# Kernel tuning notes

Hardware: AMD Instinct MI355X
Metric: run time of the kernel (lower is better)

## Reference

```python
import jax, jax.numpy as jnp
import numpy as np

N = 100000      # nodes
E = 3200000     # edges (avg degree 32)
NFEAT = 512
NHID = 256
NCLASS = 40
NLAYERS = 8
T1 = 5
T2 = 5
G1 = 1
G2 = 1
BETA = 0.5      # weight_beta
LAMDA = 0.5
ALPHA = 0.1
EPS = 1e-5


def ortho_trans(weight, T, groups):
    """Newton-Schulz orthogonalization (Ortho_Trans.forward)."""
    g = groups
    Z = weight.reshape(g, weight.shape[0] // g, -1)          # [g, d, k]
    Zc = Z - Z.mean(axis=-1, keepdims=True)
    S = jnp.einsum('gik,gjk->gij', Zc, Zc)                   # covariance [g, d, d]
    eye = jnp.eye(S.shape[-1], dtype=S.dtype)
    S = S + EPS * eye
    norm_S = jnp.sqrt(jnp.sum(S * S, axis=(1, 2), keepdims=True))  # fro norm
    S = S / norm_S
    B0 = jnp.broadcast_to(eye, S.shape)

    def body(B, _):
        B3 = B @ B @ B                                       # matrix_power3
        return 1.5 * B - 0.5 * (B3 @ S), None                # baddbmm(1.5,B,-0.5,B3,S)

    Bt, _ = jax.lax.scan(body, B0, None, length=T)
    W = (Bt @ Zc) / jnp.sqrt(norm_S)
    return W.reshape(weight.shape)


def setup_inputs() -> dict:
    key = jax.random.key(0)
    ks = jax.random.split(key, 8)
    stdv = 1.0 / np.sqrt(NHID)
    return {
        'x': jax.random.normal(ks[0], (N, NFEAT), dtype=jnp.float32),
        'edge_src': jax.random.randint(ks[1], (E,), 0, N, dtype=jnp.int32),
        'edge_dst': jax.random.randint(ks[2], (E,), 0, N, dtype=jnp.int32),
        'edge_weight': jax.random.uniform(ks[3], (E,), dtype=jnp.float32),
        'W0': jax.random.normal(ks[4], (NHID, NFEAT), dtype=jnp.float32) * 0.05,
        'b0': jnp.zeros((NHID,), dtype=jnp.float32),
        'convW': jax.random.uniform(ks[5], (NLAYERS, NHID, NHID), dtype=jnp.float32,
                                    minval=-stdv, maxval=stdv),
        'W1': jax.random.normal(ks[6], (NCLASS, NHID), dtype=jnp.float32) * 0.05,
        'b1': jnp.zeros((NCLASS,), dtype=jnp.float32),
    }


def reference(x, edge_src, edge_dst, edge_weight, W0, b0, convW, W1, b1):
    # fcs[0].weight is orthogonalized at init (Ortho=True)
    W0o = ortho_trans(W0, T1, G1)
    h = jax.nn.relu(x @ W0o.T + b0)                          # [N, NHID]
    h0 = h
    I = jnp.eye(NHID, dtype=h.dtype)
    ls = jnp.arange(1, NLAYERS + 1, dtype=h.dtype)

    def layer(h, inp):
        W, l = inp
        theta = jnp.log(LAMDA / l + 1.0)
        # sparse spmm: hi = adj @ h
        msgs = edge_weight[:, None] * h[edge_src]            # [E, NHID]
        hi = jax.ops.segment_sum(msgs, edge_dst, num_segments=N)
        support = (1.0 - ALPHA) * hi + ALPHA * h0            # variant=False -> r == support
        we = BETA * W + (1.0 - BETA) * I
        t = ortho_trans(we, T2, G2)
        out = jax.nn.relu(theta * (support @ t) + (1.0 - theta) * support)
        return out, None

    h, _ = jax.lax.scan(layer, h, (convW, ls))
    logits = h @ W1.T + b1
    return jax.nn.log_softmax(logits, axis=1)
```

## Files before the change

### kernel.cpp

```cpp
#include <hip/hip_runtime.h>
#include <math.h>

#define NNODES 100000
#define NEDGE  3200000
#define NF     512
#define NH     256
#define NC     40
#define NLAY   8
#define EPSV   1e-5f

typedef __attribute__((ext_vector_type(8))) short short8;
typedef __attribute__((ext_vector_type(4))) float floatx4;



__device__ __forceinline__ float block_sum_256(float v) {
    __shared__ float sb[8];
    #pragma unroll
    for (int off = 32; off; off >>= 1) v += __shfl_down(v, off, 64);
    if ((threadIdx.x & 63) == 0) sb[threadIdx.x >> 6] = v;
    __syncthreads();
    return sb[0] + sb[1] + sb[2] + sb[3];
}

__device__ __forceinline__ unsigned short bf16_rte(float a) {
    unsigned int u = __float_as_uint(a);
    return (unsigned short)((u + 0x7fffu + ((u >> 16) & 1u)) >> 16);
}
__device__ __forceinline__ unsigned int pack_bf2(float a, float b) {
    unsigned int ua = __float_as_uint(a), ub = __float_as_uint(b);
    ua = (ua + 0x7fffu + ((ua >> 16) & 1u)) >> 16;
    ub = (ub + 0x7fffu + ((ub >> 16) & 1u)) & 0xffff0000u;
    return ua | ub;
}


__global__ void k_hist(const int* __restrict__ dst, int* __restrict__ counts, int n) {
    int i = blockIdx.x * 256 + threadIdx.x;
    if (i < n) atomicAdd(&counts[dst[i]], 1);
}

__global__ void k_scan1(const int* __restrict__ in, int* __restrict__ out,
                        int* __restrict__ bsum, int n) {
    __shared__ int s[1024];
    int t = threadIdx.x, g = blockIdx.x * 1024 + t;
    int v = (g < n) ? in[g] : 0;
    s[t] = v; __syncthreads();
    for (int off = 1; off < 1024; off <<= 1) {
        int u = (t >= off) ? s[t - off] : 0;
        __syncthreads();
        s[t] += u;
        __syncthreads();
    }
    if (g < n) out[g] = s[t] - v;
    if (t == 1023) bsum[blockIdx.x] = s[1023];
}

__global__ void k_scan2(int* __restrict__ bsum, int nb) {
    __shared__ int s[128];
    int t = threadIdx.x;
    int v = (t < nb) ? bsum[t] : 0;
    s[t] = v; __syncthreads();
    for (int off = 1; off < 128; off <<= 1) {
        int u = (t >= off) ? s[t - off] : 0;
        __syncthreads();
        s[t] += u;
        __syncthreads();
    }
    if (t < nb) bsum[t] = s[t] - v;
}

__global__ void k_scan3(int* __restrict__ out, const int* __restrict__ bsum, int n) {
    int g = blockIdx.x * 1024 + threadIdx.x;
    if (g < n) out[g] += bsum[blockIdx.x];
}

__global__ void k_scatter(const int* __restrict__ src, const int* __restrict__ dst,
                          const float* __restrict__ w, const int* __restrict__ rstart,
                          int* __restrict__ cursor, unsigned int* __restrict__ epack, int n) {
    int i = blockIdx.x * 256 + threadIdx.x;
    if (i < n) {
        int d = dst[i];
        int pos = rstart[d] + atomicAdd(&cursor[d], 1);
        unsigned int wb = bf16_rte(w[i]) & 0x7FFFu;
        epack[pos] = ((unsigned int)src[i] << 15) | wb;
    }
}


__global__ void k_zc0(const float* __restrict__ W0, float* __restrict__ Zc0) {
    int r = blockIdx.x, t = threadIdx.x;
    float a = W0[r * NF + t];
    float b = W0[r * NF + 256 + t];
    float mean = block_sum_256(a + b) * (1.0f / 512.0f);
    Zc0[r * NF + t]       = a - mean;
    Zc0[r * NF + 256 + t] = b - mean;
}

__global__ void k_zcC(const float* __restrict__ convW, float* __restrict__ ZcC) {
    int g = blockIdx.x >> 8, r = blockIdx.x & 255, t = threadIdx.x;
    float v = 0.5f * convW[((size_t)g * NH + r) * NH + t] + ((r == t) ? 0.5f : 0.0f);
    float mean = block_sum_256(v) * (1.0f / 256.0f);
    ZcC[((size_t)g * NH + r) * NH + t] = v - mean;
}

__global__ __launch_bounds__(256) void k_gram(const float* __restrict__ Zc0,
                                              const float* __restrict__ ZcC,
                                              float* __restrict__ S) {
    const int b = blockIdx.z;
    const float* A = (b == 0) ? Zc0 : (ZcC + (size_t)(b - 1) * 65536);
    const int K = (b == 0) ? 512 : 256;
    const int r0 = blockIdx.y * 64, c0 = blockIdx.x * 64;
    __shared__ float As[32][76], Bs[32][76];
    const int t = threadIdx.x, tx = t & 15, ty = t >> 4;
    const int lr = t >> 2, lk = (t & 3) * 4;
    float acc[4][4] = {};
    for (int k0 = 0; k0 < K; k0 += 32) {
        float4 a0 = *(const float4*)(A + (size_t)(r0 + lr) * K + k0 + lk);
        float4 a1 = *(const float4*)(A + (size_t)(r0 + lr) * K + k0 + lk + 16);
        As[lk + 0][lr] = a0.x; As[lk + 1][lr] = a0.y; As[lk + 2][lr] = a0.z; As[lk + 3][lr] = a0.w;
        As[lk + 16][lr] = a1.x; As[lk + 17][lr] = a1.y; As[lk + 18][lr] = a1.z; As[lk + 19][lr] = a1.w;
        float4 b0 = *(const float4*)(A + (size_t)(c0 + lr) * K + k0 + lk);
        float4 b1 = *(const float4*)(A + (size_t)(c0 + lr) * K + k0 + lk + 16);
        Bs[lk + 0][lr] = b0.x; Bs[lk + 1][lr] = b0.y; Bs[lk + 2][lr] = b0.z; Bs[lk + 3][lr] = b0.w;
        Bs[lk + 16][lr] = b1.x; Bs[lk + 17][lr] = b1.y; Bs[lk + 18][lr] = b1.z; Bs[lk + 19][lr] = b1.w;
        __syncthreads();
        #pragma unroll
        for (int kk = 0; kk < 32; kk++) {
            float a[4], bb[4];
            *(float4*)&a[0]  = *(const float4*)&As[kk][ty * 4];
            *(float4*)&bb[0] = *(const float4*)&Bs[kk][tx * 4];
            #pragma unroll
            for (int i = 0; i < 4; i++)
                #pragma unroll
                for (int j = 0; j < 4; j++) acc[i][j] = fmaf(a[i], bb[j], acc[i][j]);
        }
        __syncthreads();
    }
    #pragma unroll
    for (int i = 0; i < 4; i++)
        #pragma unroll
        for (int j = 0; j < 4; j++) {
            int r = r0 + ty * 4 + i, c = c0 + tx * 4 + j;
            float v = acc[i][j];
            if (r == c) v += EPSV;
            S[(size_t)b * 65536 + r * NH + c] = v;
        }
}

__global__ void k_fro(const float* __restrict__ S, float* __restrict__ scales) {
    __shared__ float sb[8];
    const int b = blockIdx.x, t = threadIdx.x;
    const float* p = S + (size_t)b * 65536;
    float s = 0.f;
    for (int i = t; i < 65536; i += 256) { float v = p[i]; s = fmaf(v, v, s); }
    #pragma unroll
    for (int off = 32; off; off >>= 1) s += __shfl_down(s, off, 64);
    if ((t & 63) == 0) sb[t >> 6] = s;
    __syncthreads();
    if (t == 0) {
        float nrm = sqrtf(sb[0] + sb[1] + sb[2] + sb[3]);
        scales[b]      = 1.0f / nrm;
        scales[16 + b] = rsqrtf(nrm);
    }
}

__global__ void k_initB1(const float* __restrict__ S, const float* __restrict__ scales,
                         float* __restrict__ B) {
    int i = blockIdx.x * 256 + threadIdx.x;
    int b = i >> 16, m = i & 65535;
    float v = -0.5f * scales[b] * S[i];
    if ((m >> 8) == (m & 255)) v += 1.5f;
    B[i] = v;
}

__global__ __launch_bounds__(256) void k_ns_pair(const float* __restrict__ Bb,
                                                 const float* __restrict__ Smat,
                                                 float* __restrict__ T1b,
                                                 float* __restrict__ T2b) {
    const int b = blockIdx.z;
    const int bb = (b < 9) ? b : b - 9;
    const float* A  = Bb + (size_t)bb * 65536;
    const float* Bm = (b < 9) ? A : (Smat + (size_t)bb * 65536);
    float* C = (b < 9) ? (T1b + (size_t)bb * 65536) : (T2b + (size_t)bb * 65536);
    const int r0 = blockIdx.y * 64, c0 = blockIdx.x * 64;
    __shared__ float As[32][76], Bs[32][76];
    const int t = threadIdx.x, tx = t & 15, ty = t >> 4;
    const int lr = t >> 2, lk = (t & 3) * 4;
    const int bk = t >> 3, bc = (t & 7) * 8;
    float acc[4][4] = {};
    for (int k0 = 0; k0 < 256; k0 += 32) {
        float4 a0 = *(const float4*)(A + (size_t)(r0 + lr) * 256 + k0 + lk);
        float4 a1 = *(const float4*)(A + (size_t)(r0 + lr) * 256 + k0 + lk + 16);
        As[lk + 0][lr] = a0.x; As[lk + 1][lr] = a0.y; As[lk + 2][lr] = a0.z; As[lk + 3][lr] = a0.w;
        As[lk + 16][lr] = a1.x; As[lk + 17][lr] = a1.y; As[lk + 18][lr] = a1.z; As[lk + 19][lr] = a1.w;
        float4 b0 = *(const float4*)(Bm + (size_t)(k0 + bk) * 256 + c0 + bc);
        float4 b1 = *(const float4*)(Bm + (size_t)(k0 + bk) * 256 + c0 + bc + 4);
        *(float4*)&Bs[bk][bc]     = b0;
        *(float4*)&Bs[bk][bc + 4] = b1;
        __syncthreads();
        #pragma unroll
        for (int kk = 0; kk < 32; kk++) {
            float a[4], bb2[4];
            *(float4*)&a[0]   = *(const float4*)&As[kk][ty * 4];
            *(float4*)&bb2[0] = *(const float4*)&Bs[kk][tx * 4];
            #pragma unroll
            for (int i = 0; i < 4; i++)
                #pragma unroll
                for (int j = 0; j < 4; j++) acc[i][j] = fmaf(a[i], bb2[j], acc[i][j]);
        }
        __syncthreads();
    }
    #pragma unroll
    for (int i = 0; i < 4; i++)
        #pragma unroll
        for (int j = 0; j < 4; j++)
            C[(size_t)(r0 + ty * 4 + i) * 256 + c0 + tx * 4 + j] = acc[i][j];
}

__global__ __launch_bounds__(256) void k_small_nn(const float* __restrict__ A0,
                                                  const float* __restrict__ B0,
                                                  float* __restrict__ C0,
                                                  int sA, int sB, int sC,
                                                  int K, int Ncols, int mode,
                                                  const float* __restrict__ scale) {
    const int b = blockIdx.z;
    const float* A = A0 + (size_t)b * sA;
    const float* Bm = B0 + (size_t)b * sB;
    float* C = C0 + (size_t)b * sC;
    const int r0 = blockIdx.y * 64, c0 = blockIdx.x * 64;
    __shared__ float As[32][76], Bs[32][76];
    const int t = threadIdx.x, tx = t & 15, ty = t >> 4;
    const int lr = t >> 2, lk = (t & 3) * 4;
    const int bk = t >> 3, bc = (t & 7) * 8;
    float acc[4][4] = {};
    for (int k0 = 0; k0 < K; k0 += 32) {
        float4 a0 = *(const float4*)(A + (size_t)(r0 + lr) * K + k0 + lk);
        float4 a1 = *(const float4*)(A + (size_t)(r0 + lr) * K + k0 + lk + 16);
        As[lk + 0][lr] = a0.x; As[lk + 1][lr] = a0.y; As[lk + 2][lr] = a0.z; As[lk + 3][lr] = a0.w;
        As[lk + 16][lr] = a1.x; As[lk + 17][lr] = a1.y; As[lk + 18][lr] = a1.z; As[lk + 19][lr] = a1.w;
        float4 b0 = *(const float4*)(Bm + (size_t)(k0 + bk) * Ncols + c0 + bc);
        float4 b1 = *(const float4*)(Bm + (size_t)(k0 + bk) * Ncols + c0 + bc + 4);
        *(float4*)&Bs[bk][bc]     = b0;
        *(float4*)&Bs[bk][bc + 4] = b1;
        __syncthreads();
        #pragma unroll
        for (int kk = 0; kk < 32; kk++) {
            float a[4], bb[4];
            *(float4*)&a[0]  = *(const float4*)&As[kk][ty * 4];
            *(float4*)&bb[0] = *(const float4*)&Bs[kk][tx * 4];
            #pragma unroll
            for (int i = 0; i < 4; i++)
                #pragma unroll
                for (int j = 0; j < 4; j++) acc[i][j] = fmaf(a[i], bb[j], acc[i][j]);
        }
        __syncthreads();
    }
    #pragma unroll
    for (int i = 0; i < 4; i++)
        #pragma unroll
        for (int j = 0; j < 4; j++) {
            size_t idx = (size_t)(r0 + ty * 4 + i) * Ncols + c0 + tx * 4 + j;
            if (mode == 1) C[idx] = 1.5f * C[idx] - 0.5f * scale[b] * acc[i][j];
            else C[idx] = scale[b] * acc[i][j];
        }
}


__global__ void k_prepM(const float* __restrict__ tbuf, unsigned short* __restrict__ Mpack) {
    int idx = blockIdx.x * 256 + threadIdx.x;
    int lane = idx & 63;
    int tg   = (idx >> 6) & 15;
    int s    = (idx >> 10) & 1;
    int c    = (idx >> 11) & 3;
    int l    = idx >> 13;
    float theta = logf(0.5f / (float)(l + 1) + 1.0f);
    float mtheta = 1.0f - theta;
    int n  = tg * 16 + (lane & 15);
    int k0 = c * 64 + s * 32 + (lane >> 4) * 8;
    const float* T = tbuf + (size_t)l * 65536;
    unsigned short o[8];
    #pragma unroll
    for (int j = 0; j < 8; j++) {
        int kp = k0 + j;
        int kn = (kp & 0xC0) | ((kp & 3) << 4) | ((kp >> 2) & 15);
        float v = theta * T[(size_t)kn * 256 + n] + ((kn == n) ? mtheta : 0.0f);
        o[j] = bf16_rte(v);
    }
    *(uint4*)(Mpack + (size_t)idx * 8) = *(uint4*)o;
}

__global__ void k_prepW0(const float* __restrict__ W0o, unsigned short* __restrict__ Wpack) {
    int idx = blockIdx.x * 256 + threadIdx.x;
    int lane = idx & 63;
    int tg   = (idx >> 6) & 15;
    int s    = (idx >> 10) & 1;
    int c    = idx >> 11;
    int n  = tg * 16 + (lane & 15);
    int k0 = c * 64 + s * 32 + (lane >> 4) * 8;
    const float* p = W0o + (size_t)n * NF + k0;
    unsigned short o[8];
    #pragma unroll
    for (int j = 0; j < 8; j++) o[j] = bf16_rte(p[j]);
    *(uint4*)(Wpack + (size_t)idx * 8) = *(uint4*)o;
}



__global__ __launch_bounds__(256) void k_fc0_mfma(const float* __restrict__ X,
                                                  const unsigned short* __restrict__ Wp,
                                                  const float* __restrict__ bias,
                                                  unsigned char* __restrict__ h0u8,
                                                  float* __restrict__ h0scale) {
    __shared__ unsigned short Bs[2][16][64][8];
    __shared__ int rmax[64];
    const int t = threadIdx.x, lane = t & 63, w = t >> 6;
    const int q = lane >> 4, m = lane & 15;
    const int r0 = blockIdx.x * 64;
    if (t < 64) rmax[t] = 0;
    floatx4 acc[4][4] = {};
    for (int c = 0; c < 8; c++) {
        const uint4* src = (const uint4*)(Wp + (size_t)c * 16384);
        uint4* dst = (uint4*)&Bs[0][0][0][0];
        #pragma unroll
        for (int i = 0; i < 8; i++) dst[t + 256 * i] = src[t + 256 * i];
        __syncthreads();
        #pragma unroll
        for (int s = 0; s < 2; s++) {
            short8 afr[4];
            #pragma unroll
            for (int i = 0; i < 4; i++) {
                int row = r0 + i * 16 + m; if (row > NNODES - 1) row = NNODES - 1;
                const float* p = X + (size_t)row * NF + c * 64 + s * 32 + q * 8;
                float4 xa = *(const float4*)p;
                float4 xb = *(const float4*)(p + 4);
                uint4 af;
                af.x = pack_bf2(xa.x, xa.y); af.y = pack_bf2(xa.z, xa.w);
                af.z = pack_bf2(xb.x, xb.y); af.w = pack_bf2(xb.z, xb.w);
                afr[i] = *(short8*)&af;
            }
            #pragma unroll
            for (int tg = 0; tg < 4; tg++) {
                short8 bfr = *(const short8*)&Bs[s][w * 4 + tg][lane][0];
                #pragma unroll
                for (int i = 0; i < 4; i++)
                    acc[i][tg] = __builtin_amdgcn_mfma_f32_16x16x32_bf16(afr[i], bfr, acc[i][tg], 0, 0, 0);
            }
        }
        __syncthreads();
    }
    #pragma unroll
    for (int tg = 0; tg < 4; tg++) {
        float bv = bias[w * 64 + tg * 16 + m];
        #pragma unroll
        for (int i = 0; i < 4; i++)
            #pragma unroll
            for (int r = 0; r < 4; r++)
                acc[i][tg][r] = fmaxf(acc[i][tg][r] + bv, 0.f);
    }
    #pragma unroll
    for (int i = 0; i < 4; i++)
        #pragma unroll
        for (int r = 0; r < 4; r++) {
            float mx = fmaxf(fmaxf(acc[i][0][r], acc[i][1][r]),
                             fmaxf(acc[i][2][r], acc[i][3][r]));
            mx = fmaxf(mx, __shfl_xor(mx, 1));
            mx = fmaxf(mx, __shfl_xor(mx, 2));
            mx = fmaxf(mx, __shfl_xor(mx, 4));
            mx = fmaxf(mx, __shfl_xor(mx, 8));
            if (m == 0) atomicMax(&rmax[i * 16 + q * 4 + r], __float_as_int(mx));
        }
    __syncthreads();
    #pragma unroll
    for (int i = 0; i < 4; i++)
        #pragma unroll
        for (int r = 0; r < 4; r++) {
            int row = r0 + i * 16 + q * 4 + r;
            if (row >= NNODES) continue;
            float rm = __int_as_float(rmax[i * 16 + q * 4 + r]);
            float qs = rm > 0.f ? 255.0f / rm : 0.f;
            unsigned int b0 = (unsigned int)fmaf(acc[i][0][r], qs, 0.5f);
            unsigned int b1 = (unsigned int)fmaf(acc[i][1][r], qs, 0.5f);
            unsigned int b2 = (unsigned int)fmaf(acc[i][2][r], qs, 0.5f);
            unsigned int b3 = (unsigned int)fmaf(acc[i][3][r], qs, 0.5f);
            *(unsigned int*)(h0u8 + (size_t)row * NH + w * 64 + m * 4) =
                b0 | (b1 << 8) | (b2 << 16) | (b3 << 24);
        }
    if (t < 64 && r0 + t < NNODES)
        h0scale[r0 + t] = __int_as_float(rmax[t]) * (1.0f / 255.0f);
}


__global__ __launch_bounds__(256) void k_spmm(const int* __restrict__ rstart,
                                              const int* __restrict__ counts,
                                              const unsigned int* __restrict__ epack,
                                              const unsigned char* __restrict__ hu8,
                                              const float* __restrict__ hscale,
                                              const unsigned char* __restrict__ h0u8,
                                              const float* __restrict__ h0scale,
                                              unsigned short* __restrict__ supbf) {
    __shared__ int2 se[4][64];
    const int wv = threadIdx.x >> 6, lane = threadIdx.x & 63;
    const int node = blockIdx.x * 4 + wv;
    const int start = rstart[node], deg = counts[node];
    float a0 = 0.f, a1 = 0.f, a2 = 0.f, a3 = 0.f;
    for (int base = 0; base < deg; base += 64) {
        int j = base + lane;
        if (j < deg) {
            unsigned int u = epack[start + j];
            int s = (int)(u >> 15);
            float wt = __uint_as_float((u & 0x7FFFu) << 16);
            se[wv][lane] = make_int2(s, __float_as_int(wt * hscale[s] * 0.9f));
        }
        int mm = deg - base; if (mm > 64) mm = 64;
        int e = 0;
        for (; e + 8 <= mm; e += 8) {
            float ww[8]; unsigned int g[8];
            #pragma unroll
            for (int u = 0; u < 8; u++) {
                int2 ed = se[wv][e + u];
                ww[u] = __int_as_float(ed.y);
                g[u] = *(const unsigned int*)(hu8 + ((size_t)ed.x << 8) + (lane << 2));
            }
            #pragma unroll
            for (int u = 0; u < 8; u++) {
                a0 = fmaf(ww[u], (float)(g[u] & 0xFFu), a0);
                a1 = fmaf(ww[u], (float)((g[u] >> 8) & 0xFFu), a1);
                a2 = fmaf(ww[u], (float)((g[u] >> 16) & 0xFFu), a2);
                a3 = fmaf(ww[u], (float)(g[u] >> 24), a3);
            }
        }
        for (; e < mm; e++) {
            int2 ed = se[wv][e];
            float ww = __int_as_float(ed.y);
            unsigned int g = *(const unsigned int*)(hu8 + ((size_t)ed.x << 8) + (lane << 2));
            a0 = fmaf(ww, (float)(g & 0xFFu), a0);
            a1 = fmaf(ww, (float)((g >> 8) & 0xFFu), a1);
            a2 = fmaf(ww, (float)((g >> 16) & 0xFFu), a2);
            a3 = fmaf(ww, (float)(g >> 24), a3);
        }
    }
    unsigned int rg = *(const unsigned int*)(h0u8 + ((size_t)node << 8) + (lane << 2));
    float rs = h0scale[node] * 0.1f;
    float o0 = fmaf(rs, (float)(rg & 0xFFu), a0);
    float o1 = fmaf(rs, (float)((rg >> 8) & 0xFFu), a1);
    float o2 = fmaf(rs, (float)((rg >> 16) & 0xFFu), a2);
    float o3 = fmaf(rs, (float)(rg >> 24), a3);
    uint2 ov;
    ov.x = pack_bf2(o0, o1);
    ov.y = pack_bf2(o2, o3);
    *(uint2*)(supbf + ((size_t)node << 8) + (lane << 2)) = ov;
}


__global__ __launch_bounds__(256) void k_gemm_layer(const unsigned short* __restrict__ Sbf,
                                                    const unsigned short* __restrict__ Mp,
                                                    unsigned char* __restrict__ out_u8,
                                                    float* __restrict__ out_scale,
                                                    unsigned short* __restrict__ out_bf) {
    __shared__ int rmax[64];
    const int t = threadIdx.x, lane = t & 63, w = t >> 6;
    const int q = lane >> 4, m = lane & 15;
    const int r0 = blockIdx.x * 64;
    if (t < 64) rmax[t] = 0;
    floatx4 acc[4][4] = {};
    #pragma unroll
    for (int c = 0; c < 4; c++) {
        #pragma unroll
        for (int s = 0; s < 2; s++) {
            short8 afr[4];
            #pragma unroll
            for (int i = 0; i < 4; i++) {
                int row = r0 + i * 16 + m; if (row > NNODES - 1) row = NNODES - 1;
                afr[i] = *(const short8*)(Sbf + (size_t)row * NH + c * 64 + s * 32 + q * 8);
            }
            #pragma unroll
            for (int tg = 0; tg < 4; tg++) {
                short8 bfr = *(const short8*)(Mp + (size_t)c * 16384 + s * 8192
                                              + (w * 4 + tg) * 512 + lane * 8);
                #pragma unroll
                for (int i = 0; i < 4; i++)
                    acc[i][tg] = __builtin_amdgcn_mfma_f32_16x16x32_bf16(afr[i], bfr, acc[i][tg], 0, 0, 0);
            }
        }
    }
    #pragma unroll
    for (int i = 0; i < 4; i++)
        #pragma unroll
        for (int tg = 0; tg < 4; tg++)
            #pragma unroll
            for (int r = 0; r < 4; r++)
                acc[i][tg][r] = fmaxf(acc[i][tg][r], 0.f);

    if (out_bf) {
        #pragma unroll
        for (int i = 0; i < 4; i++)
            #pragma unroll
            for (int tg = 0; tg < 4; tg++) {
                int col = w * 64 + tg * 16 + m;
                #pragma unroll
                for (int r = 0; r < 4; r++) {
                    int row = r0 + i * 16 + q * 4 + r;
                    if (row >= NNODES) continue;
                    out_bf[(size_t)row * NH + col] = bf16_rte(acc[i][tg][r]);
                }
            }
        return;
    }
    __syncthreads();
    #pragma unroll
    for (int i = 0; i < 4; i++)
        #pragma unroll
        for (int r = 0; r < 4; r++) {
            float mx = fmaxf(fmaxf(acc[i][0][r], acc[i][1][r]),
                             fmaxf(acc[i][2][r], acc[i][3][r]));
            mx = fmaxf(mx, __shfl_xor(mx, 1));
            mx = fmaxf(mx, __shfl_xor(mx, 2));
            mx = fmaxf(mx, __shfl_xor(mx, 4));
            mx = fmaxf(mx, __shfl_xor(mx, 8));
            if (m == 0) atomicMax(&rmax[i * 16 + q * 4 + r], __float_as_int(mx));
        }
    __syncthreads();
    #pragma unroll
    for (int i = 0; i < 4; i++)
        #pragma unroll
        for (int r = 0; r < 4; r++) {
            int row = r0 + i * 16 + q * 4 + r;
            if (row >= NNODES) continue;
            float rm = __int_as_float(rmax[i * 16 + q * 4 + r]);
            float qs = rm > 0.f ? 255.0f / rm : 0.f;
            unsigned int b0 = (unsigned int)fmaf(acc[i][0][r], qs, 0.5f);
            unsigned int b1 = (unsigned int)fmaf(acc[i][1][r], qs, 0.5f);
            unsigned int b2 = (unsigned int)fmaf(acc[i][2][r], qs, 0.5f);
            unsigned int b3 = (unsigned int)fmaf(acc[i][3][r], qs, 0.5f);
            *(unsigned int*)(out_u8 + (size_t)row * NH + w * 64 + m * 4) =
                b0 | (b1 << 8) | (b2 << 16) | (b3 << 24);
        }
    if (t < 64 && r0 + t < NNODES)
        out_scale[r0 + t] = __int_as_float(rmax[t]) * (1.0f / 255.0f);
}


__global__ __launch_bounds__(128) void k_logits(const unsigned short* __restrict__ hb,
                                                const float* __restrict__ W1,
                                                const float* __restrict__ b1,
                                                float* __restrict__ out, int nrows) {
    __shared__ float hs[16][260];
    __shared__ float Ws[40][260];
    __shared__ float ls[16][44];
    __shared__ float lse[16];
    const int t = threadIdx.x;
    const int row0 = blockIdx.x * 16;
    for (int i = t; i < 40 * 64; i += 128) {
        int c = i >> 6, k4 = i & 63;
        *(float4*)&Ws[c][k4 * 4] = *(const float4*)(W1 + (size_t)c * NH + k4 * 4);
    }
    for (int i = t; i < 16 * 32; i += 128) {
        int r = i >> 5, k8 = i & 31;
        int gr = row0 + r;
        uint4 v = make_uint4(0u, 0u, 0u, 0u);
        if (gr < nrows) v = *(const uint4*)(hb + ((size_t)gr << 8) + k8 * 8);
        float* d = &hs[r][k8 * 8];
        d[0] = __uint_as_float(v.x << 16); d[1] = __uint_as_float(v.x & 0xffff0000u);
        d[2] = __uint_as_float(v.y << 16); d[3] = __uint_as_float(v.y & 0xffff0000u);
        d[4] = __uint_as_float(v.z << 16); d[5] = __uint_as_float(v.z & 0xffff0000u);
        d[6] = __uint_as_float(v.w << 16); d[7] = __uint_as_float(v.w & 0xffff0000u);
    }
    __syncthreads();
    const int r = t & 15, cg = t >> 4;
    float acc[5];
    #pragma unroll
    for (int j = 0; j < 5; j++) acc[j] = b1[cg * 5 + j];
    for (int k = 0; k < NH; k++) {
        float hv = hs[r][k];
        #pragma unroll
        for (int j = 0; j < 5; j++) acc[j] = fmaf(hv, Ws[cg * 5 + j][k], acc[j]);
    }
    #pragma unroll
    for (int j = 0; j < 5; j++) ls[r][cg * 5 + j] = acc[j];
    __syncthreads();
    if (t < 16) {
        float m = -3.4e38f;
        for (int c = 0; c < NC; c++) m = fmaxf(m, ls[t][c]);
        float s = 0.f;
        for (int c = 0; c < NC; c++) s += expf(ls[t][c] - m);
        lse[t] = m + logf(s);
    }
    __syncthreads();
    for (int i = t; i < 16 * NC; i += 128) {
        int r2 = i / NC, c = i % NC;
        int gr = row0 + r2;
        if (gr < nrows) out[(size_t)gr * NC + c] = ls[r2][c] - lse[r2];
    }
}


extern "C" void kernel_launch(void* const* d_in, const int* in_sizes, int n_in,
                              void* d_out, int out_size, void* d_ws, size_t ws_size,
                              hipStream_t stream) {
    const float* x      = (const float*)d_in[0];
    const int*   e_src  = (const int*)d_in[1];
    const int*   e_dst  = (const int*)d_in[2];
    const float* e_w    = (const float*)d_in[3];
    const float* W0     = (const float*)d_in[4];
    const float* b0     = (const float*)d_in[5];
    const float* convW  = (const float*)d_in[6];
    const float* W1     = (const float*)d_in[7];
    const float* b1     = (const float*)d_in[8];
    float* out = (float*)d_out;

    char* ws = (char*)d_ws;
    const size_t OFF_H0U8   = 0;
    const size_t OFF_HU8A   = OFF_H0U8 + (size_t)NNODES * NH;
    const size_t OFF_HU8B   = OFF_HU8A + (size_t)NNODES * NH;
    const size_t OFF_H0SC   = OFF_HU8B + (size_t)NNODES * NH;
    const size_t OFF_SCA    = OFF_H0SC + (size_t)NNODES * 4;
    const size_t OFF_SCB    = OFF_SCA + (size_t)NNODES * 4;
    const size_t OFF_SUPBF  = OFF_SCB + (size_t)NNODES * 4;
    const size_t OFF_HBF    = OFF_SUPBF + (size_t)NNODES * NH * 2;
    const size_t OFF_EPACK  = OFF_HBF + (size_t)NNODES * NH * 2;
    const size_t OFF_RSTART = OFF_EPACK + (size_t)NEDGE * 4;
    const size_t OFF_COUNTS = OFF_RSTART + (size_t)NNODES * 4;
    const size_t OFF_CURSOR = OFF_COUNTS + (size_t)NNODES * 4;
    const size_t OFF_BSUM   = OFF_CURSOR + (size_t)NNODES * 4;
    const size_t OFF_ZC0    = OFF_BSUM + 1024;
    const size_t OFF_ZCC    = OFF_ZC0 + 256 * 512 * 4;
    const size_t OFF_S      = OFF_ZCC + 8 * 65536 * 4;
    const size_t OFF_B      = OFF_S + 9 * 65536 * 4;
    const size_t OFF_T1     = OFF_B + 9 * 65536 * 4;
    const size_t OFF_T2     = OFF_T1 + 9 * 65536 * 4;
    const size_t OFF_T      = OFF_T2 + 9 * 65536 * 4;
    const size_t OFF_W0O    = OFF_T + 8 * 65536 * 4;
    const size_t OFF_SCALES = OFF_W0O + 256 * 512 * 4;
    const size_t OFF_MPACK  = OFF_SCALES + 1024;
    const size_t OFF_WPACK  = OFF_MPACK + 8 * 65536 * 2;

    unsigned char* h0u8 = (unsigned char*)(ws + OFF_H0U8);
    unsigned char* hu8A = (unsigned char*)(ws + OFF_HU8A);
    unsigned char* hu8B = (unsigned char*)(ws + OFF_HU8B);
    float* h0sc = (float*)(ws + OFF_H0SC);
    float* scA  = (float*)(ws + OFF_SCA);
    float* scB  = (float*)(ws + OFF_SCB);
    unsigned short* supbf = (unsigned short*)(ws + OFF_SUPBF);
    unsigned short* hbf   = (unsigned short*)(ws + OFF_HBF);
    unsigned int* epack  = (unsigned int*)(ws + OFF_EPACK);
    int*    rstart = (int*)(ws + OFF_RSTART);
    int*    counts = (int*)(ws + OFF_COUNTS);
    int*    cursor = (int*)(ws + OFF_CURSOR);
    int*    bsum   = (int*)(ws + OFF_BSUM);
    float*  Zc0    = (float*)(ws + OFF_ZC0);
    float*  ZcC    = (float*)(ws + OFF_ZCC);
    float*  Smat   = (float*)(ws + OFF_S);
    float*  Bb     = (float*)(ws + OFF_B);
    float*  T1b    = (float*)(ws + OFF_T1);
    float*  T2b    = (float*)(ws + OFF_T2);
    float*  tbuf   = (float*)(ws + OFF_T);
    float*  W0o    = (float*)(ws + OFF_W0O);
    float*  scales = (float*)(ws + OFF_SCALES);
    unsigned short* Mpack = (unsigned short*)(ws + OFF_MPACK);
    unsigned short* Wpack = (unsigned short*)(ws + OFF_WPACK);

    (void)in_sizes; (void)n_in; (void)out_size; (void)ws_size;

    hipMemsetAsync(counts, 0, (size_t)NNODES * 4, stream);
    hipMemsetAsync(cursor, 0, (size_t)NNODES * 4, stream);
    k_hist<<<(NEDGE + 255) / 256, 256, 0, stream>>>(e_dst, counts, NEDGE);
    const int NB = (NNODES + 1023) / 1024;
    k_scan1<<<NB, 1024, 0, stream>>>(counts, rstart, bsum, NNODES);
    k_scan2<<<1, 128, 0, stream>>>(bsum, NB);
    k_scan3<<<NB, 1024, 0, stream>>>(rstart, bsum, NNODES);
    k_scatter<<<(NEDGE + 255) / 256, 256, 0, stream>>>(e_src, e_dst, e_w, rstart, cursor,
                                                       epack, NEDGE);

    k_zc0<<<256, 256, 0, stream>>>(W0, Zc0);
    k_zcC<<<8 * 256, 256, 0, stream>>>(convW, ZcC);
    k_gram<<<dim3(4, 4, 9), 256, 0, stream>>>(Zc0, ZcC, Smat);
    k_fro<<<9, 256, 0, stream>>>(Smat, scales);
    k_initB1<<<9 * 256, 256, 0, stream>>>(Smat, scales, Bb);
    for (int it = 1; it < 5; it++) {
        k_ns_pair<<<dim3(4, 4, 18), 256, 0, stream>>>(Bb, Smat, T1b, T2b);
        k_small_nn<<<dim3(4, 4, 9), 256, 0, stream>>>(T1b, T2b, Bb, 65536, 65536, 65536,
                                                      256, 256, 1, scales);
    }
    k_small_nn<<<dim3(8, 4, 1), 256, 0, stream>>>(Bb, Zc0, W0o, 0, 0, 0,
                                                  256, 512, 2, scales + 16);
    k_small_nn<<<dim3(4, 4, 8), 256, 0, stream>>>(Bb + 65536, ZcC, tbuf, 65536, 65536, 65536,
                                                  256, 256, 2, scales + 17);

    k_prepM<<<256, 256, 0, stream>>>(tbuf, Mpack);
    k_prepW0<<<64, 256, 0, stream>>>(W0o, Wpack);

    const int GB = (NNODES + 63) / 64;
    k_fc0_mfma<<<GB, 256, 0, stream>>>(x, Wpack, b0, h0u8, h0sc);

    const unsigned char* hin = h0u8;
    const float* hinsc = h0sc;
    unsigned char* u8bufs[2] = { hu8A, hu8B };
    float* scbufs[2] = { scA, scB };
    for (int l = 1; l <= NLAY; l++) {
        k_spmm<<<NNODES / 4, 256, 0, stream>>>(rstart, counts, epack, hin, hinsc,
                                               h0u8, h0sc, supbf);
        const unsigned short* Mp = Mpack + (size_t)(l - 1) * 65536;
        if (l == NLAY) {
            k_gemm_layer<<<GB, 256, 0, stream>>>(supbf, Mp, nullptr, nullptr, hbf);
        } else {
            unsigned char* ou = u8bufs[(l - 1) & 1];
            float* os = scbufs[(l - 1) & 1];
            k_gemm_layer<<<GB, 256, 0, stream>>>(supbf, Mp, ou, os, nullptr);
            hin = ou; hinsc = os;
        }
    }

    k_logits<<<NNODES / 16, 128, 0, stream>>>(hbf, W1, b1, out, NNODES);
}
```

Baseline: 2.578 ms.

## Pre-convert X to bf16, drop LDS staging in fc0, widen logits blocks

Adds a separate kernel that converts x to bf16 in workspace, so the fc0 MFMA kernel reads bf16 A fragments directly instead of converting fp32 in-loop. It also removes the shared-memory staging of packed W0 and its barriers, loading B fragments straight from global/L2. Separately, the logits kernel processes 32 rows per 256-thread block instead of 16 per 128. The extra conversion pass writes and rereads 100MB, which may cost more than the in-kernel conversion it replaces.

```diff
diff --git a/kernel.cpp b/kernel.cpp
--- a/kernel.cpp
+++ b/kernel.cpp
@@ -85,6 +85,19 @@
         unsigned int wb = bf16_rte(w[i]) & 0x7FFFu;
         epack[pos] = ((unsigned int)src[i] << 15) | wb;
     }
+}
+
+
+__global__ void k_xbf16(const float* __restrict__ X, unsigned short* __restrict__ Xb, long n8) {
+    long i = (long)blockIdx.x * 256 + threadIdx.x;
+    if (i >= n8) return;
+    const float* p = X + i * 8;
+    float4 a = *(const float4*)p;
+    float4 b = *(const float4*)(p + 4);
+    uint4 o;
+    o.x = pack_bf2(a.x, a.y); o.y = pack_bf2(a.z, a.w);
+    o.z = pack_bf2(b.x, b.y); o.w = pack_bf2(b.z, b.w);
+    *(uint4*)(Xb + i * 8) = o;
 }
 
 
@@ -306,48 +319,36 @@
 }
 
 
-
-__global__ __launch_bounds__(256) void k_fc0_mfma(const float* __restrict__ X,
+__global__ __launch_bounds__(256) void k_fc0_mfma(const unsigned short* __restrict__ Xb,
                                                   const unsigned short* __restrict__ Wp,
                                                   const float* __restrict__ bias,
                                                   unsigned char* __restrict__ h0u8,
                                                   float* __restrict__ h0scale) {
-    __shared__ unsigned short Bs[2][16][64][8];
     __shared__ int rmax[64];
     const int t = threadIdx.x, lane = t & 63, w = t >> 6;
     const int q = lane >> 4, m = lane & 15;
     const int r0 = blockIdx.x * 64;
     if (t < 64) rmax[t] = 0;
     floatx4 acc[4][4] = {};
+    #pragma unroll
     for (int c = 0; c < 8; c++) {
-        const uint4* src = (const uint4*)(Wp + (size_t)c * 16384);
-        uint4* dst = (uint4*)&Bs[0][0][0][0];
-        #pragma unroll
-        for (int i = 0; i < 8; i++) dst[t + 256 * i] = src[t + 256 * i];
-        __syncthreads();
         #pragma unroll
         for (int s = 0; s < 2; s++) {
             short8 afr[4];
             #pragma unroll
             for (int i = 0; i < 4; i++) {
                 int row = r0 + i * 16 + m; if (row > NNODES - 1) row = NNODES - 1;
-                const float* p = X + (size_t)row * NF + c * 64 + s * 32 + q * 8;
-                float4 xa = *(const float4*)p;
-                float4 xb = *(const float4*)(p + 4);
-                uint4 af;
-                af.x = pack_bf2(xa.x, xa.y); af.y = pack_bf2(xa.z, xa.w);
-                af.z = pack_bf2(xb.x, xb.y); af.w = pack_bf2(xb.z, xb.w);
-                afr[i] = *(short8*)&af;
+                afr[i] = *(const short8*)(Xb + (size_t)row * NF + c * 64 + s * 32 + q * 8);
             }
             #pragma unroll
             for (int tg = 0; tg < 4; tg++) {
-                short8 bfr = *(const short8*)&Bs[s][w * 4 + tg][lane][0];
+                short8 bfr = *(const short8*)(Wp + (size_t)c * 16384 + s * 8192
+                                              + (w * 4 + tg) * 512 + lane * 8);
                 #pragma unroll
                 for (int i = 0; i < 4; i++)
                     acc[i][tg] = __builtin_amdgcn_mfma_f32_16x16x32_bf16(afr[i], bfr, acc[i][tg], 0, 0, 0);
             }
         }
-        __syncthreads();
     }
     #pragma unroll
     for (int tg = 0; tg < 4; tg++) {
@@ -358,6 +359,7 @@
             for (int r = 0; r < 4; r++)
                 acc[i][tg][r] = fmaxf(acc[i][tg][r] + bv, 0.f);
     }
+    __syncthreads();
     #pragma unroll
     for (int i = 0; i < 4; i++)
         #pragma unroll
@@ -541,21 +543,21 @@
 }
 
 
-__global__ __launch_bounds__(128) void k_logits(const unsigned short* __restrict__ hb,
+__global__ __launch_bounds__(256) void k_logits(const unsigned short* __restrict__ hb,
                                                 const float* __restrict__ W1,
                                                 const float* __restrict__ b1,
                                                 float* __restrict__ out, int nrows) {
-    __shared__ float hs[16][260];
+    __shared__ float hs[32][260];
     __shared__ float Ws[40][260];
-    __shared__ float ls[16][44];
-    __shared__ float lse[16];
+    __shared__ float ls[32][44];
+    __shared__ float lse[32];
     const int t = threadIdx.x;
-    const int row0 = blockIdx.x * 16;
-    for (int i = t; i < 40 * 64; i += 128) {
+    const int row0 = blockIdx.x * 32;
+    for (int i = t; i < 40 * 64; i += 256) {
         int c = i >> 6, k4 = i & 63;
         *(float4*)&Ws[c][k4 * 4] = *(const float4*)(W1 + (size_t)c * NH + k4 * 4);
     }
-    for (int i = t; i < 16 * 32; i += 128) {
+    for (int i = t; i < 32 * 32; i += 256) {
         int r = i >> 5, k8 = i & 31;
         int gr = row0 + r;
         uint4 v = make_uint4(0u, 0u, 0u, 0u);
@@ -567,7 +569,7 @@
         d[6] = __uint_as_float(v.w << 16); d[7] = __uint_as_float(v.w & 0xffff0000u);
     }
     __syncthreads();
-    const int r = t & 15, cg = t >> 4;
+    const int r = t & 31, cg = t >> 5;
     float acc[5];
     #pragma unroll
     for (int j = 0; j < 5; j++) acc[j] = b1[cg * 5 + j];
@@ -579,7 +581,7 @@
     #pragma unroll
     for (int j = 0; j < 5; j++) ls[r][cg * 5 + j] = acc[j];
     __syncthreads();
-    if (t < 16) {
+    if (t < 32) {
         float m = -3.4e38f;
         for (int c = 0; c < NC; c++) m = fmaxf(m, ls[t][c]);
         float s = 0.f;
@@ -587,7 +589,7 @@
         lse[t] = m + logf(s);
     }
     __syncthreads();
-    for (int i = t; i < 16 * NC; i += 128) {
+    for (int i = t; i < 32 * NC; i += 256) {
         int r2 = i / NC, c = i % NC;
         int gr = row0 + r2;
         if (gr < nrows) out[(size_t)gr * NC + c] = ls[r2][c] - lse[r2];
@@ -618,7 +620,8 @@
     const size_t OFF_SCB    = OFF_SCA + (size_t)NNODES * 4;
     const size_t OFF_SUPBF  = OFF_SCB + (size_t)NNODES * 4;
     const size_t OFF_HBF    = OFF_SUPBF + (size_t)NNODES * NH * 2;
-    const size_t OFF_EPACK  = OFF_HBF + (size_t)NNODES * NH * 2;
+    const size_t OFF_XBF    = OFF_HBF + (size_t)NNODES * NH * 2;
+    const size_t OFF_EPACK  = OFF_XBF + (size_t)NNODES * NF * 2;
     const size_t OFF_RSTART = OFF_EPACK + (size_t)NEDGE * 4;
     const size_t OFF_COUNTS = OFF_RSTART + (size_t)NNODES * 4;
     const size_t OFF_CURSOR = OFF_COUNTS + (size_t)NNODES * 4;
@@ -643,6 +646,7 @@
     float* scB  = (float*)(ws + OFF_SCB);
     unsigned short* supbf = (unsigned short*)(ws + OFF_SUPBF);
     unsigned short* hbf   = (unsigned short*)(ws + OFF_HBF);
+    unsigned short* xbf   = (unsigned short*)(ws + OFF_XBF);
     unsigned int* epack  = (unsigned int*)(ws + OFF_EPACK);
     int*    rstart = (int*)(ws + OFF_RSTART);
     int*    counts = (int*)(ws + OFF_COUNTS);
@@ -672,6 +676,9 @@
     k_scatter<<<(NEDGE + 255) / 256, 256, 0, stream>>>(e_src, e_dst, e_w, rstart, cursor,
                                                        epack, NEDGE);
 
+    const long N8 = (long)NNODES * NF / 8;
+    k_xbf16<<<(int)((N8 + 255) / 256), 256, 0, stream>>>(x, xbf, N8);
+
     k_zc0<<<256, 256, 0, stream>>>(W0, Zc0);
     k_zcC<<<8 * 256, 256, 0, stream>>>(convW, ZcC);
     k_gram<<<dim3(4, 4, 9), 256, 0, stream>>>(Zc0, ZcC, Smat);
@@ -691,7 +698,7 @@
     k_prepW0<<<64, 256, 0, stream>>>(W0o, Wpack);
 
     const int GB = (NNODES + 63) / 64;
-    k_fc0_mfma<<<GB, 256, 0, stream>>>(x, Wpack, b0, h0u8, h0sc);
+    k_fc0_mfma<<<GB, 256, 0, stream>>>(xbf, Wpack, b0, h0u8, h0sc);
 
     const unsigned char* hin = h0u8;
     const float* hinsc = h0sc;
@@ -711,5 +718,5 @@
         }
     }
 
-    k_logits<<<NNODES / 16, 128, 0, stream>>>(hbf, W1, b1, out, NNODES);
-}
+    k_logits<<<(NNODES + 31) / 32, 256, 0, stream>>>(hbf, W1, b1, out, NNODES);
+}
```

Measured after the change: 2.432 ms. -5.7%, faster.
